# Kernel optimization log

Hardware: AMD Instinct MI355X
Metric: run time of the kernel (lower is better)

## Reference

```python
import jax, jax.numpy as jnp
import numpy as np

EPS = 1e-12  # matches F.normalize default eps

def _angle(e):
    # e: [N, D] embeddings
    d = e[:, None, :] - e[None, :, :]                      # [N, N, D] pairwise differences
    n = jnp.linalg.norm(d, axis=-1, keepdims=True)         # [N, N, 1]
    d = d / jnp.maximum(n, EPS)                            # normalized diffs; diagonal stays 0
    # all-triplet cosines: for each anchor i, Gram matrix of its normalized diffs
    return jnp.einsum('ijd,ikd->ijk', d, d)                # [N, N, N]

def _smooth_l1_mean(a, b):
    # torch F.smooth_l1_loss with beta=1.0, reduction='mean'
    x = jnp.abs(a - b)
    return jnp.mean(jnp.where(x < 1.0, 0.5 * x * x, x - 0.5))

def setup_inputs() -> dict:
    key = jax.random.key(0)
    k1, k2 = jax.random.split(key)
    student = jax.random.normal(k1, (384, 256), dtype=jnp.float32)
    teacher = jax.random.normal(k2, (384, 256), dtype=jnp.float32)
    return {"student": student, "teacher": teacher}

def reference(student, teacher):
    s_angle = _angle(student)
    t_angle = _angle(teacher)
    return _smooth_l1_mean(s_angle, t_angle)
```

## Files before the change

### kernel.cpp

```cpp
#include <hip/hip_runtime.h>
#include <hip/hip_bf16.h>

#define NPTS 384
#define DIMS 256
#define TI 4
#define JC 48

__global__ void gram_kernel(const float* __restrict__ Es, const float* __restrict__ Et,
                            float* __restrict__ Gs, float* __restrict__ Gt) {
    const float* __restrict__ E = (blockIdx.z == 0) ? Es : Et;
    float* __restrict__ G       = (blockIdx.z == 0) ? Gs : Gt;

    __shared__ float As[32][33];
    __shared__ float Bs[32][33];

    const int tx = threadIdx.x;
    const int ty = threadIdx.y;
    const int t  = ty * 16 + tx;
    const int lr = t >> 5;
    const int lc = t & 31;
    const int i0 = blockIdx.x * 32;
    const int j0 = blockIdx.y * 32;

    float acc00 = 0.f, acc01 = 0.f, acc10 = 0.f, acc11 = 0.f;

    for (int k0 = 0; k0 < DIMS; k0 += 32) {
#pragma unroll
        for (int rr = 0; rr < 4; rr++) {
            As[lr + 8 * rr][lc] = E[(i0 + lr + 8 * rr) * DIMS + k0 + lc];
            Bs[lr + 8 * rr][lc] = E[(j0 + lr + 8 * rr) * DIMS + k0 + lc];
        }
        __syncthreads();
#pragma unroll
        for (int k = 0; k < 32; k++) {
            float a0 = As[2 * ty][k], a1 = As[2 * ty + 1][k];
            float b0 = Bs[2 * tx][k], b1 = Bs[2 * tx + 1][k];
            acc00 = fmaf(a0, b0, acc00);
            acc01 = fmaf(a0, b1, acc01);
            acc10 = fmaf(a1, b0, acc10);
            acc11 = fmaf(a1, b1, acc11);
        }
        __syncthreads();
    }

    const int i = i0 + 2 * ty;
    const int j = j0 + 2 * tx;
    G[i * NPTS + j]           = acc00;
    G[i * NPTS + j + 1]       = acc01;
    G[(i + 1) * NPTS + j]     = acc10;
    G[(i + 1) * NPTS + j + 1] = acc11;
}

__global__ void invnorm_kernel(const float* __restrict__ Gs, const float* __restrict__ Gt,
                               float* __restrict__ Rs, float* __restrict__ Rt) {
    const float* __restrict__ G = (blockIdx.y == 0) ? Gs : Gt;
    float* __restrict__ R       = (blockIdx.y == 0) ? Rs : Rt;

    int idx = blockIdx.x * 256 + threadIdx.x;
    if (idx >= NPTS * NPTS) return;
    int i = idx / NPTS;
    int j = idx - i * NPTS;

    float gii = G[i * NPTS + i];
    float gjj = G[j * NPTS + j];
    float v   = gii - 2.0f * G[idx] + gjj;
    float n   = sqrtf(fmaxf(v, 0.0f));
    float r   = 1.0f / fmaxf(n, 1e-12f);
    R[idx] = (i == j) ? 0.0f : r;
}

__global__ __launch_bounds__(NPTS) void rkd_angle_kernel(
        const float* __restrict__ Gs, const float* __restrict__ Gt,
        const float* __restrict__ Rs, const float* __restrict__ Rt,
        float* __restrict__ out) {
    __shared__ float sGs[TI][NPTS];
    __shared__ float sGt[TI][NPTS];
    __shared__ float sRs[TI][NPTS];
    __shared__ float sRt[TI][NPTS];

    const int tid = threadIdx.x;
    const int i0  = blockIdx.x * TI;
    const int j0  = blockIdx.y * JC;

#pragma unroll
    for (int r = 0; r < TI; r++) {
        int row = (i0 + r) * NPTS;
        sGs[r][tid] = Gs[row + tid];
        sGt[r][tid] = Gt[row + tid];
        sRs[r][tid] = Rs[row + tid];
        sRt[r][tid] = Rt[row + tid];
    }
    __syncthreads();

    const int k = tid;
    float gii_s[TI], gii_t[TI], rik_s[TI], rik_t[TI], qik_s[TI], qik_t[TI];
#pragma unroll
    for (int r = 0; r < TI; r++) {
        gii_s[r] = sGs[r][i0 + r];
        gii_t[r] = sGt[r][i0 + r];
        rik_s[r] = sRs[r][k];
        rik_t[r] = sRt[r][k];
        qik_s[r] = rik_s[r] * sGs[r][k];
        qik_t[r] = rik_t[r] * sGt[r][k];
    }

    float acc = 0.0f;
    for (int j = j0; j < j0 + JC; j++) {
        float gs_jk = Gs[j * NPTS + k];
        float gt_jk = Gt[j * NPTS + k];
#pragma unroll
        for (int r = 0; r < TI; r++) {
            float cs = gii_s[r] - sGs[r][j];
            float as = sRs[r][j] * fmaf(rik_s[r], gs_jk + cs, -qik_s[r]);
            float ct = gii_t[r] - sGt[r][j];
            float at = sRt[r][j] * fmaf(rik_t[r], gt_jk + ct, -qik_t[r]);
            float x  = fabsf(as - at);
            acc += (x < 1.0f) ? 0.5f * x * x : x - 0.5f;
        }
    }

#pragma unroll
    for (int off = 32; off > 0; off >>= 1)
        acc += __shfl_down(acc, off, 64);

    __shared__ float wsum[NPTS / 64];
    const int wid  = tid >> 6;
    const int lane = tid & 63;
    if (lane == 0) wsum[wid] = acc;
    __syncthreads();
    if (tid == 0) {
        float s = 0.0f;
#pragma unroll
        for (int w = 0; w < NPTS / 64; w++) s += wsum[w];
        atomicAdd(out, s * (1.0f / (384.0f * 384.0f * 384.0f)));
    }
}

extern "C" void kernel_launch(void* const* d_in, const int* in_sizes, int n_in,
                              void* d_out, int out_size, void* d_ws, size_t ws_size,
                              hipStream_t stream) {
    const float* student = (const float*)d_in[0];
    const float* teacher = (const float*)d_in[1];
    float* out = (float*)d_out;

    float* Gs = (float*)d_ws;
    float* Gt = Gs + NPTS * NPTS;
    float* Rs = Gt + NPTS * NPTS;
    float* Rt = Rs + NPTS * NPTS;

    hipMemsetAsync(d_out, 0, sizeof(float), stream);

    dim3 ggrid(NPTS / 32, NPTS / 32, 2);
    dim3 gblock(16, 16, 1);
    gram_kernel<<<ggrid, gblock, 0, stream>>>(student, teacher, Gs, Gt);

    dim3 ngrid((NPTS * NPTS + 255) / 256, 2, 1);
    invnorm_kernel<<<ngrid, 256, 0, stream>>>(Gs, Gt, Rs, Rt);

    dim3 mgrid(NPTS / TI, NPTS / JC, 1);
    rkd_angle_kernel<<<mgrid, NPTS, 0, stream>>>(Gs, Gt, Rs, Rt, out);
}
```

Baseline: 103.6 us.

## Fuse inverse-norm into Gram kernel, precompute squared norms, streamline main loop

Adds a prep kernel that computes row squared norms and zeroes the output in place of the memset. The Gram kernel drops shared-memory tiling for direct float4 global loads and now writes the inverse distance and the gii-gij term as a packed float2 pair, which removes the separate invnorm kernel. The main kernel no longer stages rows in shared memory and reads the packed pairs from global memory instead. The smooth-L1 branch is replaced by a med3-based form, and two accumulators are used. The risk is heavier global or L2 traffic in the Gram kernel without shared-memory reuse, plus broadcast global loads in the inner loop.

```diff
diff --git a/kernel.cpp b/kernel.cpp
--- a/kernel.cpp
+++ b/kernel.cpp
@@ -6,129 +6,131 @@
 #define TI 4
 #define JC 48
 
-__global__ void gram_kernel(const float* __restrict__ Es, const float* __restrict__ Et,
-                            float* __restrict__ Gs, float* __restrict__ Gt) {
-    const float* __restrict__ E = (blockIdx.z == 0) ? Es : Et;
-    float* __restrict__ G       = (blockIdx.z == 0) ? Gs : Gt;
+__global__ __launch_bounds__(256) void prep_kernel(
+        const float* __restrict__ Es, const float* __restrict__ Et,
+        float* __restrict__ sqn , float* __restrict__ out) {
+    const float* __restrict__ E = (blockIdx.y == 0) ? Es : Et;
+    const int wave = threadIdx.x >> 6;
+    const int lane = threadIdx.x & 63;
+    const int row  = blockIdx.x * 4 + wave;
 
-    __shared__ float As[32][33];
-    __shared__ float Bs[32][33];
+    const float4 v = ((const float4*)(E + row * DIMS))[lane];
+    float s = v.x * v.x + v.y * v.y + v.z * v.z + v.w * v.w;
+#pragma unroll
+    for (int off = 32; off > 0; off >>= 1)
+        s += __shfl_down(s, off, 64);
+    if (lane == 0) sqn[blockIdx.y * NPTS + row] = s;
+    if (blockIdx.x == 0 && blockIdx.y == 0 && threadIdx.x == 0) out[0] = 0.0f;
+}
+
+__global__ __launch_bounds__(256) void gram_kernel(
+        const float* __restrict__ Es, const float* __restrict__ Et,
+        const float* __restrict__ sqn,
+        float* __restrict__ Gs, float* __restrict__ Gt,
+        float2* __restrict__ RCs, float2* __restrict__ RCt) {
+    const int z = blockIdx.z;
+    const float* __restrict__ E  = z ? Et : Es;
+    float*       __restrict__ G  = z ? Gt : Gs;
+    float2*      __restrict__ RC = z ? RCt : RCs;
+    const float* __restrict__ sq = sqn + z * NPTS;
 
     const int tx = threadIdx.x;
     const int ty = threadIdx.y;
-    const int t  = ty * 16 + tx;
-    const int lr = t >> 5;
-    const int lc = t & 31;
-    const int i0 = blockIdx.x * 32;
-    const int j0 = blockIdx.y * 32;
+    const int i  = blockIdx.x * 32 + 2 * ty;
+    const int j  = blockIdx.y * 32 + 2 * tx;
 
-    float acc00 = 0.f, acc01 = 0.f, acc10 = 0.f, acc11 = 0.f;
+    const float4* __restrict__ a0 = (const float4*)(E + i * DIMS);
+    const float4* __restrict__ a1 = (const float4*)(E + (i + 1) * DIMS);
+    const float4* __restrict__ b0 = (const float4*)(E + j * DIMS);
+    const float4* __restrict__ b1 = (const float4*)(E + (j + 1) * DIMS);
 
-    for (int k0 = 0; k0 < DIMS; k0 += 32) {
-#pragma unroll
-        for (int rr = 0; rr < 4; rr++) {
-            As[lr + 8 * rr][lc] = E[(i0 + lr + 8 * rr) * DIMS + k0 + lc];
-            Bs[lr + 8 * rr][lc] = E[(j0 + lr + 8 * rr) * DIMS + k0 + lc];
-        }
-        __syncthreads();
-#pragma unroll
-        for (int k = 0; k < 32; k++) {
-            float a0 = As[2 * ty][k], a1 = As[2 * ty + 1][k];
-            float b0 = Bs[2 * tx][k], b1 = Bs[2 * tx + 1][k];
-            acc00 = fmaf(a0, b0, acc00);
-            acc01 = fmaf(a0, b1, acc01);
-            acc10 = fmaf(a1, b0, acc10);
-            acc11 = fmaf(a1, b1, acc11);
-        }
-        __syncthreads();
+    float g00 = 0.f, g01 = 0.f, g10 = 0.f, g11 = 0.f;
+#pragma unroll 8
+    for (int k = 0; k < DIMS / 4; k++) {
+        float4 av0 = a0[k], av1 = a1[k], bv0 = b0[k], bv1 = b1[k];
+        g00 = fmaf(av0.x, bv0.x, g00); g00 = fmaf(av0.y, bv0.y, g00);
+        g00 = fmaf(av0.z, bv0.z, g00); g00 = fmaf(av0.w, bv0.w, g00);
+        g01 = fmaf(av0.x, bv1.x, g01); g01 = fmaf(av0.y, bv1.y, g01);
+        g01 = fmaf(av0.z, bv1.z, g01); g01 = fmaf(av0.w, bv1.w, g01);
+        g10 = fmaf(av1.x, bv0.x, g10); g10 = fmaf(av1.y, bv0.y, g10);
+        g10 = fmaf(av1.z, bv0.z, g10); g10 = fmaf(av1.w, bv0.w, g10);
+        g11 = fmaf(av1.x, bv1.x, g11); g11 = fmaf(av1.y, bv1.y, g11);
+        g11 = fmaf(av1.z, bv1.z, g11); g11 = fmaf(av1.w, bv1.w, g11);
     }
 
-    const int i = i0 + 2 * ty;
-    const int j = j0 + 2 * tx;
-    G[i * NPTS + j]           = acc00;
-    G[i * NPTS + j + 1]       = acc01;
-    G[(i + 1) * NPTS + j]     = acc10;
-    G[(i + 1) * NPTS + j + 1] = acc11;
+    const float sii0 = sq[i], sii1 = sq[i + 1];
+    const float sjj0 = sq[j], sjj1 = sq[j + 1];
+
+    float g[2][2] = {{g00, g01}, {g10, g11}};
+    float si[2] = {sii0, sii1};
+    float sj[2] = {sjj0, sjj1};
+#pragma unroll
+    for (int r = 0; r < 2; r++) {
+#pragma unroll
+        for (int c = 0; c < 2; c++) {
+            int ii = i + r, jj = j + c;
+            float gv = g[r][c];
+            float v  = si[r] + sj[c] - 2.0f * gv;
+            float n  = sqrtf(fmaxf(v, 0.0f));
+            float rr = (ii == jj) ? 0.0f : (1.0f / fmaxf(n, 1e-12f));
+            G[ii * NPTS + jj]  = gv;
+            RC[ii * NPTS + jj] = make_float2(rr, si[r] - gv);
+        }
+    }
 }
 
-__global__ void invnorm_kernel(const float* __restrict__ Gs, const float* __restrict__ Gt,
-                               float* __restrict__ Rs, float* __restrict__ Rt) {
-    const float* __restrict__ G = (blockIdx.y == 0) ? Gs : Gt;
-    float* __restrict__ R       = (blockIdx.y == 0) ? Rs : Rt;
+__global__ __launch_bounds__(NPTS) void rkd_main_kernel(
+        const float* __restrict__ Gs, const float* __restrict__ Gt,
+        const float2* __restrict__ RCs, const float2* __restrict__ RCt,
+        float* __restrict__ out) {
+    const int k  = threadIdx.x;
+    const int i0 = blockIdx.x * TI;
+    const int j0 = blockIdx.y * JC;
 
-    int idx = blockIdx.x * 256 + threadIdx.x;
-    if (idx >= NPTS * NPTS) return;
-    int i = idx / NPTS;
-    int j = idx - i * NPTS;
-
-    float gii = G[i * NPTS + i];
-    float gjj = G[j * NPTS + j];
-    float v   = gii - 2.0f * G[idx] + gjj;
-    float n   = sqrtf(fmaxf(v, 0.0f));
-    float r   = 1.0f / fmaxf(n, 1e-12f);
-    R[idx] = (i == j) ? 0.0f : r;
-}
-
-__global__ __launch_bounds__(NPTS) void rkd_angle_kernel(
-        const float* __restrict__ Gs, const float* __restrict__ Gt,
-        const float* __restrict__ Rs, const float* __restrict__ Rt,
-        float* __restrict__ out) {
-    __shared__ float sGs[TI][NPTS];
-    __shared__ float sGt[TI][NPTS];
-    __shared__ float sRs[TI][NPTS];
-    __shared__ float sRt[TI][NPTS];
-
-    const int tid = threadIdx.x;
-    const int i0  = blockIdx.x * TI;
-    const int j0  = blockIdx.y * JC;
-
+    float ru_s[TI], vu_s[TI], ru_t[TI], vu_t[TI];
 #pragma unroll
     for (int r = 0; r < TI; r++) {
-        int row = (i0 + r) * NPTS;
-        sGs[r][tid] = Gs[row + tid];
-        sGt[r][tid] = Gt[row + tid];
-        sRs[r][tid] = Rs[row + tid];
-        sRt[r][tid] = Rt[row + tid];
-    }
-    __syncthreads();
-
-    const int k = tid;
-    float gii_s[TI], gii_t[TI], rik_s[TI], rik_t[TI], qik_s[TI], qik_t[TI];
-#pragma unroll
-    for (int r = 0; r < TI; r++) {
-        gii_s[r] = sGs[r][i0 + r];
-        gii_t[r] = sGt[r][i0 + r];
-        rik_s[r] = sRs[r][k];
-        rik_t[r] = sRt[r][k];
-        qik_s[r] = rik_s[r] * sGs[r][k];
-        qik_t[r] = rik_t[r] * sGt[r][k];
+        const int row = (i0 + r) * NPTS + k;
+        float rs = RCs[row].x, gs = Gs[row];
+        float rt = RCt[row].x, gt = Gt[row];
+        ru_s[r] = rs; vu_s[r] = -rs * gs;
+        ru_t[r] = rt; vu_t[r] = -rt * gt;
     }
 
-    float acc = 0.0f;
-    for (int j = j0; j < j0 + JC; j++) {
-        float gs_jk = Gs[j * NPTS + k];
-        float gt_jk = Gt[j * NPTS + k];
+    float acc0 = 0.0f, acc1 = 0.0f;
+#pragma unroll 2
+    for (int jj = 0; jj < JC; jj++) {
+        const int j = j0 + jj;
+        const float gjs = Gs[j * NPTS + k];
+        const float gjt = Gt[j * NPTS + k];
 #pragma unroll
         for (int r = 0; r < TI; r++) {
-            float cs = gii_s[r] - sGs[r][j];
-            float as = sRs[r][j] * fmaf(rik_s[r], gs_jk + cs, -qik_s[r]);
-            float ct = gii_t[r] - sGt[r][j];
-            float at = sRt[r][j] * fmaf(rik_t[r], gt_jk + ct, -qik_t[r]);
-            float x  = fabsf(as - at);
-            acc += (x < 1.0f) ? 0.5f * x * x : x - 0.5f;
+            const int row = (i0 + r) * NPTS + j;
+            const float2 pcs = RCs[row];
+            const float2 pct = RCt[row];
+            float ws = fmaf(ru_s[r], gjs + pcs.y, vu_s[r]);
+            float wt = fmaf(ru_t[r], gjt + pct.y, vu_t[r]);
+            float mt = pct.x * wt;
+            float d  = fmaf(pcs.x, ws, -mt);
+            float q  = d * d;
+            float u  = fmaf(2.0f, fabsf(d), -1.0f);
+            float m  = __builtin_amdgcn_fmed3f(q, u, 1.0f);
+            if (r & 1) acc1 = fmaf(0.5f, m, acc1);
+            else       acc0 = fmaf(0.5f, m, acc0);
         }
     }
 
+    float acc = acc0 + acc1;
 #pragma unroll
     for (int off = 32; off > 0; off >>= 1)
         acc += __shfl_down(acc, off, 64);
 
     __shared__ float wsum[NPTS / 64];
-    const int wid  = tid >> 6;
-    const int lane = tid & 63;
+    const int wid  = k >> 6;
+    const int lane = k & 63;
     if (lane == 0) wsum[wid] = acc;
     __syncthreads();
-    if (tid == 0) {
+    if (k == 0) {
         float s = 0.0f;
 #pragma unroll
         for (int w = 0; w < NPTS / 64; w++) s += wsum[w];
@@ -143,20 +145,17 @@
     const float* teacher = (const float*)d_in[1];
     float* out = (float*)d_out;
 
-    float* Gs = (float*)d_ws;
-    float* Gt = Gs + NPTS * NPTS;
-    float* Rs = Gt + NPTS * NPTS;
-    float* Rt = Rs + NPTS * NPTS;
+    float*  Gs  = (float*)d_ws;
+    float*  Gt  = Gs + NPTS * NPTS;
+    float2* RCs = (float2*)(Gt + NPTS * NPTS);
+    float2* RCt = RCs + NPTS * NPTS;
+    float*  sqn = (float*)(RCt + NPTS * NPTS);
 
-    hipMemsetAsync(d_out, 0, sizeof(float), stream);
+    prep_kernel<<<dim3(NPTS / 4, 2), 256, 0, stream>>>(student, teacher, sqn, out);
 
-    dim3 ggrid(NPTS / 32, NPTS / 32, 2);
-    dim3 gblock(16, 16, 1);
-    gram_kernel<<<ggrid, gblock, 0, stream>>>(student, teacher, Gs, Gt);
+    gram_kernel<<<dim3(NPTS / 32, NPTS / 32, 2), dim3(16, 16), 0, stream>>>(
+        student, teacher, sqn, Gs, Gt, RCs, RCt);
 
-    dim3 ngrid((NPTS * NPTS + 255) / 256, 2, 1);
-    invnorm_kernel<<<ngrid, 256, 0, stream>>>(Gs, Gt, Rs, Rt);
-
-    dim3 mgrid(NPTS / TI, NPTS / JC, 1);
-    rkd_angle_kernel<<<mgrid, NPTS, 0, stream>>>(Gs, Gt, Rs, Rt, out);
+    rkd_main_kernel<<<dim3(NPTS / TI, NPTS / JC), NPTS, 0, stream>>>(
+        Gs, Gt, RCs, RCt, out);
 }
```

Measured after the change: 117.9 us. 13.9% more time.
